# Kernel tuning notes

Hardware: AMD Instinct MI355X
Metric: run time of the kernel (lower is better)

Reference implementation:

```python
import jax, jax.numpy as jnp
import numpy as np

D_MODEL = 1024
HEADS = 16
D_K = D_MODEL // HEADS


def setup_inputs() -> dict:
    key = jax.random.key(0)
    ks = jax.random.split(key, 11)
    B, S = 4, 2048
    scale = 1.0 / np.sqrt(D_MODEL)
    return {
        "q": jax.random.normal(ks[0], (B, S, D_MODEL), jnp.float32),
        "k": jax.random.normal(ks[1], (B, S, D_MODEL), jnp.float32),
        "v": jax.random.normal(ks[2], (B, S, D_MODEL), jnp.float32),
        "wq": jax.random.normal(ks[3], (D_MODEL, D_MODEL), jnp.float32) * scale,
        "bq": jax.random.normal(ks[4], (D_MODEL,), jnp.float32) * 0.01,
        "wk": jax.random.normal(ks[5], (D_MODEL, D_MODEL), jnp.float32) * scale,
        "bk": jax.random.normal(ks[6], (D_MODEL,), jnp.float32) * 0.01,
        "wv": jax.random.normal(ks[7], (D_MODEL, D_MODEL), jnp.float32) * scale,
        "bv": jax.random.normal(ks[8], (D_MODEL,), jnp.float32) * 0.01,
        "wo": jax.random.normal(ks[9], (D_MODEL, D_MODEL), jnp.float32) * scale,
        "bo": jax.random.normal(ks[10], (D_MODEL,), jnp.float32) * 0.01,
    }


def reference(q, k, v, wq, bq, wk, bk, wv, bv, wo, bo):
    B, S, _ = q.shape
    # nn.Linear: x @ W^T + b
    qp = q @ wq.T + bq
    kp = k @ wk.T + bk
    vp = v @ wv.T + bv
    # [B, S, D] -> [B, H, S, d_k]
    def split_heads(x):
        return x.reshape(B, S, HEADS, D_K).transpose(0, 2, 1, 3)
    qh, kh, vh = split_heads(qp), split_heads(kp), split_heads(vp)
    # scaled dot-product attention (dropout p=0 -> identity)
    scores = jnp.einsum("bhsd,bhtd->bhst", qh, kh) / jnp.sqrt(jnp.float32(D_K)).astype(qh.dtype)
    attn = jax.nn.softmax(scores, axis=-1)
    ctx = jnp.einsum("bhst,bhtd->bhsd", attn, vh)
    # merge heads and output projection
    ctx = ctx.transpose(0, 2, 1, 3).reshape(B, S, D_MODEL)
    return ctx @ wo.T + bo
```

## Files before the change

kernel.cpp:

```cpp
#include <hip/hip_runtime.h>


typedef __attribute__((ext_vector_type(8))) short bf16x8;
typedef __attribute__((ext_vector_type(4))) float f32x4;
typedef unsigned int u32;

#define DEVI __device__ __forceinline__

static constexpr int S_LEN = 2048;
static constexpr int NH = 16;
static constexpr int DK = 64;
static constexpr float Q_SCALE = 0.125f * 1.44269504088896340736f;

DEVI unsigned short f2b(float f) {
    unsigned int u = __builtin_bit_cast(unsigned int, f);
    u += 0x7fffu + ((u >> 16) & 1u);
    return (unsigned short)(u >> 16);
}

DEVI u32 pkbf16(float a, float b) {
#if __has_builtin(__builtin_amdgcn_cvt_pk_bf16_f32)
    auto r = __builtin_amdgcn_cvt_pk_bf16_f32(a, b);
    return __builtin_bit_cast(u32, r);
#else
    return (u32)f2b(a) | ((u32)f2b(b) << 16);
#endif
}

DEVI float fexp2(float x) {
#if __has_builtin(__builtin_amdgcn_exp2f)
    return __builtin_amdgcn_exp2f(x);
#else
    return exp2f(x);
#endif
}

DEVI f32x4 mfma16(bf16x8 a, bf16x8 b, f32x4 c) {
    return __builtin_amdgcn_mfma_f32_16x16x32_bf16(a, b, c, 0, 0, 0);
}

#define GLL16(g, l)                                                        \
    __builtin_amdgcn_global_load_lds(                                      \
        (const __attribute__((address_space(1))) u32*)(g),                 \
        (__attribute__((address_space(3))) u32*)(l), 16, 0, 0)

#define SBAR __builtin_amdgcn_sched_barrier(0)
#define PHB  SBAR; __builtin_amdgcn_s_barrier(); SBAR

__global__ __launch_bounds__(256) void cvt_all(
    const float* __restrict__ q, const float* __restrict__ k,
    const float* __restrict__ v, const float* __restrict__ wq,
    const float* __restrict__ wk, const float* __restrict__ wv,
    const float* __restrict__ wo, unsigned short* __restrict__ dq,
    unsigned short* __restrict__ dk, unsigned short* __restrict__ dv,
    unsigned short* __restrict__ wb) {
    const int id = blockIdx.x;
    const float* src;
    unsigned short* dst;
    long i;
    if (id < 12288) {
        int z = id >> 12, x = id & 4095;
        src = z == 0 ? q : z == 1 ? k : v;
        dst = z == 0 ? dq : z == 1 ? dk : dv;
        i = ((long)x * 256 + threadIdx.x) * 8;
    } else {
        int wi = id - 12288;
        int z = wi >> 9, x = wi & 511;
        src = z == 0 ? wq : z == 1 ? wk : z == 2 ? wv : wo;
        dst = wb + (long)z * 1048576;
        i = ((long)x * 256 + threadIdx.x) * 8;
    }
    float4 v0 = *(const float4*)(src + i);
    float4 v1 = *(const float4*)(src + i + 4);
    uint4 o;
    o.x = pkbf16(v0.x, v0.y);
    o.y = pkbf16(v0.z, v0.w);
    o.z = pkbf16(v1.x, v1.y);
    o.w = pkbf16(v1.z, v1.w);
    *(uint4*)(dst + i) = o;
}

#define MM16(MH)                                                           \
    __builtin_amdgcn_s_setprio(1);                                         \
    _Pragma("unroll") for (int mi = 0; mi < 4; ++mi)                       \
        _Pragma("unroll") for (int ni = 0; ni < 2; ++ni)                   \
            _Pragma("unroll") for (int kk = 0; kk < 2; ++kk)               \
                acc[(MH)*4 + mi][ni] = mfma16(                             \
                    a[mi][kk], b[ni][kk], acc[(MH)*4 + mi][ni]);           \
    __builtin_amdgcn_s_setprio(0);

DEVI void gemm_core(const unsigned short* __restrict__ Am,
                    const unsigned short* __restrict__ Wm,
                    int m0, int n0, int tid, f32x4 (&acc)[8][2]) {
    __shared__ __align__(16) unsigned short As[2][256 * 64];
    __shared__ __align__(16) unsigned short Bs[2][128 * 64];
    const int wid = tid >> 6, l = tid & 63, l16 = l & 15, quad = l >> 4;
    const int swz = l16 & 7;
    const int wm = (wid >> 2) * 128, wn = (wid & 3) * 32;
    unsigned short *As0 = &As[0][0], *As1 = &As[1][0];
    unsigned short *Bs0 = &Bs[0][0], *Bs1 = &Bs[1][0];

    bf16x8 a[4][2], b[2][2];

    auto stg = [&](const unsigned short* Mat, int r0, int ko,
                   unsigned short* lds, int type) {
        #pragma unroll
        for (int pass = 0; pass < 2; ++pass) {
            int wlr = pass * 64 + wid * 8;
            int row0 = type == 0 ? (wlr < 64 ? wlr : wlr + 64)
                     : type == 1 ? 64 + (wlr < 64 ? wlr : wlr + 64)
                                 : wlr;
            int row = row0 + (l >> 3);
            int cl = (l & 7) ^ (l >> 3);
            GLL16(Mat + (long)(r0 + row) * 1024 + ko + cl * 8, lds + row0 * 64);
        }
    };
    auto lda = [&](const unsigned short* as, int mh) {
        #pragma unroll
        for (int mi = 0; mi < 4; ++mi)
            #pragma unroll
            for (int kk = 0; kk < 2; ++kk)
                a[mi][kk] = *(const bf16x8*)(as +
                    (wm + (mh * 4 + mi) * 16 + l16) * 64 +
                    (((kk * 4 + quad) ^ swz) << 3));
    };
    auto ldb = [&](const unsigned short* bs) {
        #pragma unroll
        for (int ni = 0; ni < 2; ++ni)
            #pragma unroll
            for (int kk = 0; kk < 2; ++kk)
                b[ni][kk] = *(const bf16x8*)(bs +
                    (wn + ni * 16 + l16) * 64 +
                    (((kk * 4 + quad) ^ swz) << 3));
    };

    stg(Am, m0, 0, As0, 0);
    stg(Wm, n0, 0, Bs0, 2);
    stg(Am, m0, 0, As0, 1);
    stg(Am, m0, 64, As1, 0);
    asm volatile("s_waitcnt vmcnt(2)" ::: "memory");
    __builtin_amdgcn_s_barrier(); SBAR;

    #pragma unroll 1
    for (int it = 0; it < 8; ++it) {
        const bool F = it < 7;
        const int ko1 = it * 128 + 64, ko2 = it * 128 + 128, ko3 = it * 128 + 192;
        lda(As0, 0); ldb(Bs0);
        stg(Wm, n0, ko1, Bs1, 2);
        stg(Am, m0, ko1, As1, 1);
        PHB; MM16(0); PHB;
        lda(As0, 1);
        if (F) stg(Am, m0, ko2, As0, 0);
        PHB; MM16(1);
        SBAR;
        if (F) { asm volatile("s_waitcnt vmcnt(2)" ::: "memory"); }
        else   { asm volatile("s_waitcnt vmcnt(0)" ::: "memory"); }
        __builtin_amdgcn_s_barrier(); SBAR;
        lda(As1, 0); ldb(Bs1);
        if (F) { stg(Wm, n0, ko2, Bs0, 2); stg(Am, m0, ko2, As0, 1); }
        PHB; MM16(0); PHB;
        lda(As1, 1);
        if (F) stg(Am, m0, ko3, As1, 0);
        PHB; MM16(1);
        SBAR;
        if (F) { asm volatile("s_waitcnt vmcnt(2)" ::: "memory"); }
        __builtin_amdgcn_s_barrier(); SBAR;
    }
}

DEVI void gemm_bid(int& m0, int& n0) {
    int bid = blockIdx.y * 8 + blockIdx.x;
    int b2 = (bid & 7) * 32 + (bid >> 3);
    m0 = (b2 >> 3) * 256;
    n0 = (b2 & 7) * 128;
}

__global__ __launch_bounds__(512, 2) void gemm_qkv(
    const unsigned short* __restrict__ aq, const unsigned short* __restrict__ ak,
    const unsigned short* __restrict__ av, const unsigned short* __restrict__ wqkv,
    const float* __restrict__ bq, const float* __restrict__ bk,
    const float* __restrict__ bv, unsigned short* __restrict__ qh,
    unsigned short* __restrict__ kh, unsigned short* __restrict__ vht) {
    const int tid = threadIdx.x;
    const int wid = tid >> 6, l = tid & 63, l16 = l & 15, quad = l >> 4;
    const int wm = (wid >> 2) * 128, wn = (wid & 3) * 32;
    int m0, n0;
    gemm_bid(m0, n0);
    const int z = blockIdx.z;
    const unsigned short* Am = z == 0 ? aq : z == 1 ? ak : av;
    const unsigned short* Wm = wqkv + (long)z * 1048576;
    const float* bias = z == 0 ? bq : z == 1 ? bk : bv;

    f32x4 acc[8][2] = {};
    gemm_core(Am, Wm, m0, n0, tid, acc);

    if (z < 2) {
        unsigned short* out = z == 0 ? qh : kh;
        const float scale = z == 0 ? Q_SCALE : 1.0f;
        #pragma unroll
        for (int ni = 0; ni < 2; ++ni) {
            int n = n0 + wn + ni * 16 + l16;
            float bvl = bias[n];
            int hh = n >> 6, dd = n & 63;
            #pragma unroll
            for (int mi = 0; mi < 8; ++mi)
                #pragma unroll
                for (int r = 0; r < 4; ++r) {
                    int m = m0 + wm + mi * 16 + quad * 4 + r;
                    int bb = m >> 11, ss = m & 2047;
                    out[(((long)(bb * NH + hh) * S_LEN + ss) * DK) + dd] =
                        f2b((acc[mi][ni][r] + bvl) * scale);
                }
        }
    } else {
        #pragma unroll
        for (int ni = 0; ni < 2; ++ni) {
            int n = n0 + wn + ni * 16 + l16;
            float bvl = bias[n];
            int hh = n >> 6, dd = n & 63;
            #pragma unroll
            for (int mi = 0; mi < 8; ++mi) {
                int m = m0 + wm + mi * 16 + quad * 4;
                int bb = m >> 11, ss = m & 2047;
                uint2 pk;
                pk.x = pkbf16(acc[mi][ni][0] + bvl, acc[mi][ni][1] + bvl);
                pk.y = pkbf16(acc[mi][ni][2] + bvl, acc[mi][ni][3] + bvl);
                *(uint2*)(vht + ((long)(bb * NH + hh) * DK + dd) * S_LEN + ss) = pk;
            }
        }
    }
}

__global__ __launch_bounds__(512, 2) void gemm_out(
    const unsigned short* __restrict__ A, const unsigned short* __restrict__ W,
    const float* __restrict__ bias, float* __restrict__ out) {
    const int tid = threadIdx.x;
    const int wid = tid >> 6, l = tid & 63, l16 = l & 15, quad = l >> 4;
    const int wm = (wid >> 2) * 128, wn = (wid & 3) * 32;
    int m0, n0;
    gemm_bid(m0, n0);

    f32x4 acc[8][2] = {};
    gemm_core(A, W, m0, n0, tid, acc);

    #pragma unroll
    for (int ni = 0; ni < 2; ++ni) {
        int n = n0 + wn + ni * 16 + l16;
        float bv = bias[n];
        #pragma unroll
        for (int mi = 0; mi < 8; ++mi)
            #pragma unroll
            for (int r = 0; r < 4; ++r) {
                int m = m0 + wm + mi * 16 + quad * 4 + r;
                out[(long)m * 1024 + n] = acc[mi][ni][r] + bv;
            }
    }
}

__global__ __launch_bounds__(256, 3) void attn(
    const unsigned short* __restrict__ qh, const unsigned short* __restrict__ kh,
    const unsigned short* __restrict__ vht, unsigned short* __restrict__ ctx) {
    __shared__ __align__(16) unsigned short Kb[2][4096];
    __shared__ __align__(16) unsigned short Vb[3][4096];
    __shared__ __align__(16) unsigned short P[128 * 44];

    const int id = blockIdx.y * 16 + blockIdx.x;
    const int id2 = (id & 7) * 128 + (id >> 3);
    const int qt = id2 & 15, bh = id2 >> 4;
    const int tid = threadIdx.x;
    const int w = tid >> 6, l = tid & 63, l16 = l & 15, quad = l >> 4;

    const unsigned short* kh_b = kh + (long)bh * 2048 * 64;
    const unsigned short* vh_b = vht + (long)bh * 64 * 2048;

    const unsigned short* qsrc = qh + ((long)bh * 2048 + qt * 128) * 64;
    bf16x8 qf[2][2];
    #pragma unroll
    for (int dd = 0; dd < 2; ++dd)
        #pragma unroll
        for (int i = 0; i < 2; ++i)
            qf[dd][i] = *(const bf16x8*)(qsrc + (w * 32 + i * 16 + l16) * 64 +
                                         dd * 32 + quad * 8);
    #pragma unroll
    for (int dd = 0; dd < 2; ++dd)
        #pragma unroll
        for (int i = 0; i < 2; ++i)
            asm volatile("" :: "v"(qf[dd][i]));

    auto stage_k = [&](const unsigned short* base, int buf) {
        #pragma unroll
        for (int rr = 0; rr < 2; ++rr) {
            int sb = rr * 256 + w * 64;
            int slot = sb + l;
            int row = slot >> 3, cc = (slot & 7) ^ (row & 7);
            GLL16(base + (long)row * 64 + cc * 8, &Kb[buf][sb * 8]);
        }
    };
    auto stage_v = [&](const unsigned short* vbase, int buf) {
        #pragma unroll
        for (int rr = 0; rr < 2; ++rr) {
            int sb = rr * 256 + w * 64;
            int slot = sb + l;
            int d = slot >> 3, cc = (slot & 7) ^ (d & 7);
            GLL16(vbase + (long)d * 2048 + cc * 8, &Vb[buf][sb * 8]);
        }
    };

    stage_k(kh_b, 0);
    stage_v(vh_b, 0);
    stage_v(vh_b + 64, 1);
    asm volatile("s_waitcnt vmcnt(2)" ::: "memory");
    __builtin_amdgcn_s_barrier();
    __builtin_amdgcn_sched_barrier(0);

    f32x4 o[4][2] = {};
    f32x4 osum[2] = {};
    bf16x8 ones;
    #pragma unroll
    for (int j = 0; j < 8; ++j) ones[j] = (short)0x3f80;

    const unsigned short* kstage = kh_b + 64 * 64;
    const unsigned short* vstage = vh_b + 2 * 64;
    int vr = 0, vs = 2;
    for (int kt = 0; kt < 32; ++kt) {
        if (kt < 31) stage_k(kstage, (kt + 1) & 1);
        if (kt < 30) stage_v(vstage, vs);
        kstage += 64 * 64;
        vstage += 64;
        __builtin_amdgcn_sched_barrier(0);

        const unsigned short* kb = Kb[kt & 1];
        f32x4 sa[2][4] = {};
        #pragma unroll
        for (int dd = 0; dd < 2; ++dd) {
            bf16x8 kf[4];
            #pragma unroll
            for (int ja = 0; ja < 4; ++ja) {
                int row = ja * 16 + l16;
                kf[ja] = *(const bf16x8*)(kb + (row * 8 + ((dd * 4 + quad) ^ (row & 7))) * 8);
            }
            __builtin_amdgcn_s_setprio(1);
            #pragma unroll
            for (int i = 0; i < 2; ++i)
                #pragma unroll
                for (int ja = 0; ja < 4; ++ja)
                    sa[i][ja] = mfma16(kf[ja], qf[dd][i], sa[i][ja]);
            __builtin_amdgcn_s_setprio(0);
        }

        #pragma unroll
        for (int i = 0; i < 2; ++i)
            #pragma unroll
            for (int ja = 0; ja < 4; ++ja)
                #pragma unroll
                for (int r = 0; r < 4; ++r)
                    sa[i][ja][r] = fexp2(sa[i][ja][r]);

        const unsigned short* vb = Vb[vr];
        #pragma unroll
        for (int qtr = 0; qtr < 2; ++qtr) {
            #pragma unroll
            for (int jh = 0; jh < 2; ++jh)
                #pragma unroll
                for (int i = 0; i < 2; ++i) {
                    int row = w * 32 + i * 16 + l16;
                    int ja = qtr * 2 + jh;
                    uint2 pk;
                    pk.x = pkbf16(sa[i][ja][0], sa[i][ja][1]);
                    pk.y = pkbf16(sa[i][ja][2], sa[i][ja][3]);
                    *(uint2*)(&P[row * 44 + jh * 16 + quad * 4]) = pk;
                }
            bf16x8 vf[4], pf[2];
            #pragma unroll
            for (int jd = 0; jd < 4; ++jd) {
                int d = jd * 16 + l16;
                vf[jd] = *(const bf16x8*)(vb + (d * 8 + ((qtr * 4 + quad) ^ (d & 7))) * 8);
            }
            #pragma unroll
            for (int i = 0; i < 2; ++i) {
                int row = w * 32 + i * 16 + l16;
                pf[i] = *(const bf16x8*)(&P[row * 44 + quad * 8]);
            }
            __builtin_amdgcn_s_setprio(1);
            #pragma unroll
            for (int jd = 0; jd < 4; ++jd)
                #pragma unroll
                for (int i = 0; i < 2; ++i)
                    o[jd][i] = mfma16(vf[jd], pf[i], o[jd][i]);
            #pragma unroll
            for (int i = 0; i < 2; ++i)
                osum[i] = mfma16(ones, pf[i], osum[i]);
            __builtin_amdgcn_s_setprio(0);
        }

        if (kt < 30) {
            asm volatile("s_waitcnt vmcnt(2)" ::: "memory");
        } else if (kt == 30) {
            asm volatile("s_waitcnt vmcnt(0)" ::: "memory");
        }
        if (kt < 31) {
            __builtin_amdgcn_s_barrier();
            __builtin_amdgcn_sched_barrier(0);
        }

        vr = (vr + 1 == 3) ? 0 : vr + 1;
        vs = (vs + 1 == 3) ? 0 : vs + 1;
    }

    const int b = bh >> 4, hh = bh & 15;
    #pragma unroll
    for (int i = 0; i < 2; ++i) {
        float inv = 1.0f / osum[i][0];
        int s = qt * 128 + w * 32 + i * 16 + l16;
        #pragma unroll
        for (int jd = 0; jd < 4; ++jd) {
            uint2 pk;
            pk.x = pkbf16(o[jd][i][0] * inv, o[jd][i][1] * inv);
            pk.y = pkbf16(o[jd][i][2] * inv, o[jd][i][3] * inv);
            *(uint2*)(&ctx[((long)(b * 2048 + s) * 1024) + hh * 64 + jd * 16 + quad * 4]) = pk;
        }
    }
}

extern "C" void kernel_launch(void* const* d_in, const int* in_sizes, int n_in,
                              void* d_out, int out_size, void* d_ws, size_t ws_size,
                              hipStream_t stream) {
    const float* q  = (const float*)d_in[0];
    const float* k  = (const float*)d_in[1];
    const float* v  = (const float*)d_in[2];
    const float* wq = (const float*)d_in[3];
    const float* bq = (const float*)d_in[4];
    const float* wk = (const float*)d_in[5];
    const float* bk = (const float*)d_in[6];
    const float* wv = (const float*)d_in[7];
    const float* bv = (const float*)d_in[8];
    const float* wo = (const float*)d_in[9];
    const float* bo = (const float*)d_in[10];
    float* out = (float*)d_out;

    const size_t NE = 8u * 1024u * 1024u;
    unsigned short* ab_q = (unsigned short*)d_ws;
    unsigned short* qh   = ab_q + NE;
    unsigned short* kh   = qh + NE;
    unsigned short* vht  = kh + NE;
    unsigned short* wb   = vht + NE;
    unsigned short* wob  = wb + 3 * 1048576;
    unsigned short* ctx  = ab_q;
    unsigned short* ab_k = (unsigned short*)d_out;
    unsigned short* ab_v = ab_k + NE;

    cvt_all<<<dim3(14336), dim3(256), 0, stream>>>(q, k, v, wq, wk, wv, wo,
                                                   ab_q, ab_k, ab_v, wb);
    gemm_qkv<<<dim3(8, 32, 3), dim3(512), 0, stream>>>(ab_q, ab_k, ab_v, wb,
                                                       bq, bk, bv, qh, kh, vht);
    attn<<<dim3(16, 64), dim3(256), 0, stream>>>(qh, kh, vht, ctx);
    gemm_out<<<dim3(8, 32), dim3(512), 0, stream>>>(ctx, wob, bo, out);
}
```

Measured before the change: 345.7 us.

## Fuse fp32-to-bf16 activation conversion into QKV GEMM A-tile loading

Removes the separate conversion pass over q/k/v activations and keeps only the weight conversion kernel. The QKV GEMM now loads fp32 A tiles into registers, converts them to bf16 and writes them to swizzled LDS, staged with a reworked register/LDS double-buffer schedule. This avoids writing and re-reading the bf16 activation copies (about 100MB of traffic) and one kernel launch. In exchange the GEMM reads twice as many bytes for A, uses more registers for staging and can no longer use async global-to-LDS loads for A, which may expose load latency.

```diff
diff --git a/kernel.cpp b/kernel.cpp
--- a/kernel.cpp
+++ b/kernel.cpp
@@ -46,38 +46,24 @@
 
 #define SBAR __builtin_amdgcn_sched_barrier(0)
 #define PHB  SBAR; __builtin_amdgcn_s_barrier(); SBAR
-
-__global__ __launch_bounds__(256) void cvt_all(
-    const float* __restrict__ q, const float* __restrict__ k,
-    const float* __restrict__ v, const float* __restrict__ wq,
-    const float* __restrict__ wk, const float* __restrict__ wv,
-    const float* __restrict__ wo, unsigned short* __restrict__ dq,
-    unsigned short* __restrict__ dk, unsigned short* __restrict__ dv,
-    unsigned short* __restrict__ wb) {
-    const int id = blockIdx.x;
-    const float* src;
-    unsigned short* dst;
-    long i;
-    if (id < 12288) {
-        int z = id >> 12, x = id & 4095;
-        src = z == 0 ? q : z == 1 ? k : v;
-        dst = z == 0 ? dq : z == 1 ? dk : dv;
-        i = ((long)x * 256 + threadIdx.x) * 8;
-    } else {
-        int wi = id - 12288;
-        int z = wi >> 9, x = wi & 511;
-        src = z == 0 ? wq : z == 1 ? wk : z == 2 ? wv : wo;
-        dst = wb + (long)z * 1048576;
-        i = ((long)x * 256 + threadIdx.x) * 8;
-    }
+#define LGKM0 asm volatile("s_waitcnt lgkmcnt(0)" ::: "memory")
+
+__global__ __launch_bounds__(256) void cvt_w(
+    const float* __restrict__ a, const float* __restrict__ b,
+    const float* __restrict__ c, const float* __restrict__ d,
+    unsigned short* __restrict__ o) {
+    const float* src = blockIdx.y == 0 ? a : blockIdx.y == 1 ? b
+                     : blockIdx.y == 2 ? c : d;
+    unsigned short* dst = o + (long)blockIdx.y * 1048576;
+    long i = ((long)blockIdx.x * 256 + threadIdx.x) * 8;
     float4 v0 = *(const float4*)(src + i);
     float4 v1 = *(const float4*)(src + i + 4);
-    uint4 o;
-    o.x = pkbf16(v0.x, v0.y);
-    o.y = pkbf16(v0.z, v0.w);
-    o.z = pkbf16(v1.x, v1.y);
-    o.w = pkbf16(v1.z, v1.w);
-    *(uint4*)(dst + i) = o;
+    uint4 ov;
+    ov.x = pkbf16(v0.x, v0.y);
+    ov.y = pkbf16(v0.z, v0.w);
+    ov.z = pkbf16(v1.x, v1.y);
+    ov.w = pkbf16(v1.z, v1.w);
+    *(uint4*)(dst + i) = ov;
 }
 
 #define MM16(MH)                                                           \
@@ -168,6 +154,116 @@
     }
 }
 
+DEVI void gemm_core_f32a(const float* __restrict__ Am,
+                         const unsigned short* __restrict__ Wm,
+                         int m0, int n0, int tid, f32x4 (&acc)[8][2]) {
+    __shared__ __align__(16) unsigned short As[2][256 * 64];
+    __shared__ __align__(16) unsigned short Bs[2][128 * 64];
+    const int wid = tid >> 6, l = tid & 63, l16 = l & 15, quad = l >> 4;
+    const int swz = l16 & 7;
+    const int wm = (wid >> 2) * 128, wn = (wid & 3) * 32;
+    unsigned short *As0 = &As[0][0], *As1 = &As[1][0];
+    unsigned short *Bs0 = &Bs[0][0], *Bs1 = &Bs[1][0];
+
+    bf16x8 a[4][2], b[2][2];
+    float4 rgA[2][2], rgB[2][2];
+
+    auto issA = [&](int ko, int type, float4 (&rg)[2][2]) {
+        #pragma unroll
+        for (int pass = 0; pass < 2; ++pass) {
+            int wlr = pass * 64 + wid * 8;
+            int row0 = (type ? 64 : 0) + (wlr < 64 ? wlr : wlr + 64);
+            int row = row0 + (l >> 3);
+            int cl = (l & 7) ^ (l >> 3);
+            const float* p = Am + (long)(m0 + row) * 1024 + ko + cl * 8;
+            rg[pass][0] = *(const float4*)(p);
+            rg[pass][1] = *(const float4*)(p + 4);
+        }
+    };
+    auto wrA = [&](unsigned short* lds, int type, float4 (&rg)[2][2]) {
+        #pragma unroll
+        for (int pass = 0; pass < 2; ++pass) {
+            int wlr = pass * 64 + wid * 8;
+            int row0 = (type ? 64 : 0) + (wlr < 64 ? wlr : wlr + 64);
+            uint4 o;
+            o.x = pkbf16(rg[pass][0].x, rg[pass][0].y);
+            o.y = pkbf16(rg[pass][0].z, rg[pass][0].w);
+            o.z = pkbf16(rg[pass][1].x, rg[pass][1].y);
+            o.w = pkbf16(rg[pass][1].z, rg[pass][1].w);
+            *(uint4*)(lds + row0 * 64 + l * 8) = o;
+        }
+    };
+    auto stgB = [&](int ko, unsigned short* lds) {
+        #pragma unroll
+        for (int pass = 0; pass < 2; ++pass) {
+            int wlr = pass * 64 + wid * 8;
+            int row = wlr + (l >> 3);
+            int cl = (l & 7) ^ (l >> 3);
+            GLL16(Wm + (long)(n0 + row) * 1024 + ko + cl * 8, lds + wlr * 64);
+        }
+    };
+    auto lda = [&](const unsigned short* as, int mh) {
+        #pragma unroll
+        for (int mi = 0; mi < 4; ++mi)
+            #pragma unroll
+            for (int kk = 0; kk < 2; ++kk)
+                a[mi][kk] = *(const bf16x8*)(as +
+                    (wm + (mh * 4 + mi) * 16 + l16) * 64 +
+                    (((kk * 4 + quad) ^ swz) << 3));
+    };
+    auto ldb = [&](const unsigned short* bs) {
+        #pragma unroll
+        for (int ni = 0; ni < 2; ++ni)
+            #pragma unroll
+            for (int kk = 0; kk < 2; ++kk)
+                b[ni][kk] = *(const bf16x8*)(bs +
+                    (wn + ni * 16 + l16) * 64 +
+                    (((kk * 4 + quad) ^ swz) << 3));
+    };
+
+    issA(0, 0, rgA);
+    issA(0, 1, rgB);
+    stgB(0, Bs0);
+    wrA(As0, 0, rgA);
+    wrA(As0, 1, rgB);
+    issA(64, 0, rgA);
+    wrA(As1, 0, rgA);
+    issA(64, 1, rgB);
+    LGKM0;
+    __builtin_amdgcn_s_barrier(); SBAR;
+
+    #pragma unroll 1
+    for (int it = 0; it < 8; ++it) {
+        const bool F = it < 7;
+        const int ko1 = it * 128 + 64, ko2 = it * 128 + 128, ko3 = it * 128 + 192;
+        wrA(As1, 1, rgB);
+        if (F) issA(ko2, 0, rgA);
+        stgB(ko1, Bs1);
+        lda(As0, 0); ldb(Bs0);
+        LGKM0;
+        PHB; MM16(0); PHB;
+        if (F) { wrA(As0, 0, rgA); issA(ko2, 1, rgB); }
+        lda(As0, 1);
+        LGKM0;
+        PHB; MM16(1);
+        SBAR;
+        if (F) { asm volatile("s_waitcnt vmcnt(4)" ::: "memory"); }
+        else   { asm volatile("s_waitcnt vmcnt(0)" ::: "memory"); }
+        __builtin_amdgcn_s_barrier(); SBAR;
+        if (F) { wrA(As0, 1, rgB); issA(ko3, 0, rgA); stgB(ko2, Bs0); }
+        lda(As1, 0); ldb(Bs1);
+        LGKM0;
+        PHB; MM16(0); PHB;
+        if (F) { wrA(As1, 0, rgA); issA(ko3, 1, rgB); }
+        lda(As1, 1);
+        LGKM0;
+        PHB; MM16(1);
+        SBAR;
+        if (F) { asm volatile("s_waitcnt vmcnt(4)" ::: "memory"); }
+        __builtin_amdgcn_s_barrier(); SBAR;
+    }
+}
+
 DEVI void gemm_bid(int& m0, int& n0) {
     int bid = blockIdx.y * 8 + blockIdx.x;
     int b2 = (bid & 7) * 32 + (bid >> 3);
@@ -176,8 +272,8 @@
 }
 
 __global__ __launch_bounds__(512, 2) void gemm_qkv(
-    const unsigned short* __restrict__ aq, const unsigned short* __restrict__ ak,
-    const unsigned short* __restrict__ av, const unsigned short* __restrict__ wqkv,
+    const float* __restrict__ q, const float* __restrict__ k,
+    const float* __restrict__ v, const unsigned short* __restrict__ wqkv,
     const float* __restrict__ bq, const float* __restrict__ bk,
     const float* __restrict__ bv, unsigned short* __restrict__ qh,
     unsigned short* __restrict__ kh, unsigned short* __restrict__ vht) {
@@ -187,12 +283,12 @@
     int m0, n0;
     gemm_bid(m0, n0);
     const int z = blockIdx.z;
-    const unsigned short* Am = z == 0 ? aq : z == 1 ? ak : av;
+    const float* Am = z == 0 ? q : z == 1 ? k : v;
     const unsigned short* Wm = wqkv + (long)z * 1048576;
     const float* bias = z == 0 ? bq : z == 1 ? bk : bv;
 
     f32x4 acc[8][2] = {};
-    gemm_core(Am, Wm, m0, n0, tid, acc);
+    gemm_core_f32a(Am, Wm, m0, n0, tid, acc);
 
     if (z < 2) {
         unsigned short* out = z == 0 ? qh : kh;
@@ -439,19 +535,15 @@
     float* out = (float*)d_out;
 
     const size_t NE = 8u * 1024u * 1024u;
-    unsigned short* ab_q = (unsigned short*)d_ws;
-    unsigned short* qh   = ab_q + NE;
+    unsigned short* ctx  = (unsigned short*)d_ws;
+    unsigned short* qh   = ctx + NE;
     unsigned short* kh   = qh + NE;
     unsigned short* vht  = kh + NE;
     unsigned short* wb   = vht + NE;
     unsigned short* wob  = wb + 3 * 1048576;
-    unsigned short* ctx  = ab_q;
-    unsigned short* ab_k = (unsigned short*)d_out;
-    unsigned short* ab_v = ab_k + NE;
-
-    cvt_all<<<dim3(14336), dim3(256), 0, stream>>>(q, k, v, wq, wk, wv, wo,
-                                                   ab_q, ab_k, ab_v, wb);
-    gemm_qkv<<<dim3(8, 32, 3), dim3(512), 0, stream>>>(ab_q, ab_k, ab_v, wb,
+
+    cvt_w<<<dim3(512, 4), dim3(256), 0, stream>>>(wq, wk, wv, wo, wb);
+    gemm_qkv<<<dim3(8, 32, 3), dim3(512), 0, stream>>>(q, k, v, wb,
                                                        bq, bk, bv, qh, kh, vht);
     attn<<<dim3(16, 64), dim3(256), 0, stream>>>(qh, kh, vht, ctx);
     gemm_out<<<dim3(8, 32), dim3(512), 0, stream>>>(ctx, wob, bo, out);
```

New measurement: 392.7 us. +13.6%, slower.
